# Kernel tuning notes

Measured on AMD Instinct MI355X. Metric: run time of the kernel, lower is better.

The kernel has to match this reference:

```python
import jax, jax.numpy as jnp
import numpy as np
import itertools, string

# Weight space: 2-layer MLP params, flattened in dict-key order (W1, W2, b1, b2).
SPECS = [(0, 1), (1, 2), (1,), (2,)]
N = 1024            # size of each permutable dim (perm ids 0,1,2)
C_IN, C_OUT = 16, 16
NUM_TERMS = [9, 10, 7, 6]   # equivariant basis terms per output leaf


def _set_partitions(elems):
    if not elems:
        yield []
        return
    first, rest = elems[0], elems[1:]
    for part in _set_partitions(rest):
        for i in range(len(part)):
            yield part[:i] + [part[i] + [first]] + part[i + 1:]
        yield part + [[first]]


def gen_basis(out_spec, in_spec, out_dims, x):
    """All permutation-equivariant basis maps from x (*in_dims, c) to (*out_dims, c).
    Basis elements <-> set partitions of (in,out) axis positions sharing a perm id:
    in-axes in a block are diagonalized; in-only blocks are summed; mixed blocks copy
    the axis to the matching out position; out-only blocks broadcast."""
    pos = ([('in', a, p) for a, p in enumerate(in_spec)]
           + [('out', a, p) for a, p in enumerate(out_spec)])
    by_pid = {}
    for q in pos:
        by_pid.setdefault(q[2], []).append(q)
    parts = [list(_set_partitions(by_pid[p])) for p in sorted(by_pid)]
    terms = []
    for combo in itertools.product(*parts):
        blocks = [b for part in combo for b in part]
        pos2b = {(q[0], q[1]): bi for bi, b in enumerate(blocks) for q in b}
        L = string.ascii_lowercase
        in_sub = ''.join(L[pos2b[('in', a)]] for a in range(len(in_spec)))
        mixed = [bi for bi, b in enumerate(blocks)
                 if any(q[0] == 'in' for q in b) and any(q[0] == 'out' for q in b)]
        out_sub = ''.join(L[bi] for bi in mixed)
        # diagonal over repeated in-axes, sum over in-only blocks; z = channel axis
        t = jnp.einsum(f'{in_sub}z->{out_sub}z', x)
        targets = [min(q[1] for q in blocks[bi] if q[0] == 'out') for bi in mixed]
        t = jnp.transpose(t, list(np.argsort(targets)) + [len(mixed)])
        st = sorted(targets)
        for ax in range(len(out_dims)):
            if ax not in st:
                t = jnp.expand_dims(t, ax)
        t = jnp.broadcast_to(t, tuple(out_dims) + (x.shape[-1],))
        for b in blocks:  # diagonal-embed blocks with >1 out axis (not hit for MLP specs)
            outs = sorted(q[1] for q in b if q[0] == 'out')
            for a1, a2 in zip(outs, outs[1:]):
                n = out_dims[a1]
                sh = [1] * (len(out_dims) + 1)
                sh[a1] = n; sh[a2] = n
                t = t * jnp.eye(n, dtype=x.dtype).reshape(sh)
        terms.append(t)
    return terms


def _forward(flat, thetas, biases):
    outs = []
    for i in range(len(flat)):
        out_dims = flat[i].shape[:-1]
        acc = jnp.zeros(tuple(out_dims) + (C_OUT,), dtype=flat[i].dtype)
        k = 0
        for j in range(len(flat)):
            for term in gen_basis(SPECS[i], SPECS[j], out_dims, flat[j]):
                acc = acc + jnp.einsum('...i,io->...o', term, thetas[i][k])
                k += 1
        outs.append(acc + biases[i])
    return tuple(outs)


def setup_inputs() -> dict:
    key = jax.random.key(0)
    ks = jax.random.split(key, 12)
    inp = {
        'W1': jax.random.normal(ks[0], (N, N, C_IN), jnp.float32),
        'W2': jax.random.normal(ks[1], (N, N, C_IN), jnp.float32),
        'b1': jax.random.normal(ks[2], (N, C_IN), jnp.float32),
        'b2': jax.random.normal(ks[3], (N, C_IN), jnp.float32),
    }
    for i, k in enumerate(NUM_TERMS):
        scale = (1.0 / (C_IN * k)) ** 0.5
        inp[f'theta_{i}'] = scale * jax.random.normal(ks[4 + i], (k, C_IN, C_OUT), jnp.float32)
        inp[f'bias_{i}'] = jnp.zeros((C_OUT,), jnp.float32)
    return inp


def reference(W1, W2, b1, b2, theta_0, theta_1, theta_2, theta_3,
              bias_0, bias_1, bias_2, bias_3):
    return _forward([W1, W2, b1, b2],
                    [theta_0, theta_1, theta_2, theta_3],
                    [bias_0, bias_1, bias_2, bias_3])
```

## Files before the change

### kernel.cpp

```cpp
#include <hip/hip_runtime.h>

#define NDIM 1024
#define CH 16
#define ROW_FLOATS (NDIM * CH)
#define ROW_F4 (ROW_FLOATS / 4)

__device__ inline float4 f4add(float4 a, float4 b) {
    return make_float4(a.x + b.x, a.y + b.y, a.z + b.z, a.w + b.w);
}

__global__ __launch_bounds__(256) void k_fused(const float* __restrict__ W1,
                                               const float* __restrict__ W2,
                                               float* __restrict__ rowpart,
                                               float* __restrict__ colpart) {
    int t  = threadIdx.x;
    int jt = blockIdx.x, it = blockIdx.y, z = blockIdx.z;
    int i0 = it * 16, j0 = jt * 64;
    const float4* Wf4 = (const float4*)(z ? W2 : W1);
    const float4* base = Wf4 + (size_t)i0 * ROW_F4 + jt * 256 + t;

    __shared__ float4 tile[16][257];
    float4 colacc = make_float4(0.f, 0.f, 0.f, 0.f);
#pragma unroll
    for (int r = 0; r < 16; ++r) {
        float4 v = base[(size_t)r * ROW_F4];
        colacc = f4add(colacc, v);
        tile[r][t] = v;
    }
    ((float4*)colpart)[(((size_t)z * 64 + it) * NDIM + j0) * 4 + t] = colacc;
    __syncthreads();
    if (t < 64) {
        int r = t >> 2, cq = t & 3;
        float4 s = make_float4(0.f, 0.f, 0.f, 0.f);
#pragma unroll
        for (int jl = 0; jl < 64; ++jl) s = f4add(s, tile[r][jl * 4 + cq]);
        ((float4*)rowpart)[(((size_t)z * 16 + jt) * NDIM + (i0 + r)) * 4 + cq] = s;
    }
}

__global__ __launch_bounds__(256) void k_finalize(const float* __restrict__ rowpart,
                                                  const float* __restrict__ colpart,
                                                  float* __restrict__ rowsumF,
                                                  float* __restrict__ colsumF) {
    int gt = blockIdx.x * 256 + threadIdx.x;
    if (gt < 32768) {
        int z = gt >> 14, idx = gt & 16383;
        const float* p = rowpart + (size_t)z * 16 * 16384 + idx;
        float s = 0.f;
#pragma unroll
        for (int c = 0; c < 16; ++c) s += p[(size_t)c * 16384];
        rowsumF[gt] = s;
    } else {
        int rem = gt - 32768;
        int z = rem >> 14, idx = rem & 16383;
        const float* p = colpart + (size_t)z * 64 * 16384 + idx;
        float s = 0.f;
#pragma unroll
        for (int c = 0; c < 64; ++c) s += p[(size_t)c * 16384];
        colsumF[rem] = s;
    }
}

__global__ __launch_bounds__(256) void k_sums(const float* __restrict__ rowsum,
                                              const float* __restrict__ b1,
                                              const float* __restrict__ b2,
                                              float* __restrict__ sums) {
    int tgt = blockIdx.x;
    const float* src = (tgt == 0) ? rowsum
                     : (tgt == 1) ? rowsum + 16384
                     : (tgt == 2) ? b1 : b2;
    int t = threadIdx.x;
    const float4* s4 = (const float4*)src;
    float4 a = make_float4(0.f, 0.f, 0.f, 0.f);
#pragma unroll
    for (int k = 0; k < 16; ++k) a = f4add(a, s4[t + 256 * k]);
    __shared__ float4 lds[256];
    lds[t] = a;
    __syncthreads();
    if (t < 64) {
        float4 s = lds[t];
#pragma unroll
        for (int o = 1; o < 4; ++o) s = f4add(s, lds[t + 64 * o]);
        lds[t] = s;
    }
    __syncthreads();
    if (t < 4) {
        float4 s = make_float4(0.f, 0.f, 0.f, 0.f);
#pragma unroll
        for (int m = 0; m < 16; ++m) s = f4add(s, lds[t + 4 * m]);
        float* dst = sums + tgt * 16 + 4 * t;
        dst[0] = s.x; dst[1] = s.y; dst[2] = s.z; dst[3] = s.w;
    }
}

__global__ __launch_bounds__(256) void k_smalls(const float* __restrict__ rowsum,
                                                const float* __restrict__ colsum,
                                                const float* __restrict__ sums,
                                                const float* __restrict__ b1,
                                                const float* __restrict__ b2,
                                                const float* __restrict__ th0,
                                                const float* __restrict__ th1,
                                                const float* __restrict__ th2,
                                                const float* __restrict__ th3,
                                                const float* __restrict__ bias0,
                                                const float* __restrict__ bias1,
                                                const float* __restrict__ bias2,
                                                const float* __restrict__ bias3,
                                                float* __restrict__ R0, float* __restrict__ C0,
                                                float* __restrict__ R1, float* __restrict__ C1,
                                                float* __restrict__ out2, float* __restrict__ out3) {
    int gt = blockIdx.x * 256 + threadIdx.x;
    int i = gt >> 4, o = gt & 15;
    const float* rs1 = rowsum + i * 16;
    const float* rs2 = rowsum + 16384 + i * 16;
    const float* cs1 = colsum + i * 16;
    const float* cs2 = colsum + 16384 + i * 16;
    const float* b1i = b1 + i * 16;
    const float* b2i = b2 + i * 16;
    float r0 = 0.f, c0a = 0.f, r1 = 0.f, c1a = 0.f, o2 = 0.f, o3 = 0.f;
    float k0 = 0.f, k1 = 0.f, k2 = 0.f, k3 = 0.f;
#pragma unroll
    for (int c = 0; c < 16; ++c) {
        float sW1 = sums[c], sW2 = sums[16 + c], sb1 = sums[32 + c], sb2 = sums[48 + c];
        r0  += rs1[c] * th0[(1 * 16 + c) * 16 + o];
        c0a += cs1[c] * th0[(2 * 16 + c) * 16 + o]
             + rs2[c] * th0[(4 * 16 + c) * 16 + o]
             + b1i[c] * th0[(6 * 16 + c) * 16 + o];
        k0  += sW1 * th0[(3 * 16 + c) * 16 + o] + sW2 * th0[(5 * 16 + c) * 16 + o]
             + sb1 * th0[(7 * 16 + c) * 16 + o] + sb2 * th0[(8 * 16 + c) * 16 + o];
        r1  += cs1[c] * th1[(0 * 16 + c) * 16 + o]
             + rs2[c] * th1[(3 * 16 + c) * 16 + o]
             + b1i[c] * th1[(6 * 16 + c) * 16 + o];
        c1a += cs2[c] * th1[(4 * 16 + c) * 16 + o]
             + b2i[c] * th1[(8 * 16 + c) * 16 + o];
        k1  += sW1 * th1[(1 * 16 + c) * 16 + o] + sW2 * th1[(5 * 16 + c) * 16 + o]
             + sb1 * th1[(7 * 16 + c) * 16 + o] + sb2 * th1[(9 * 16 + c) * 16 + o];
        o2  += cs1[c] * th2[(0 * 16 + c) * 16 + o]
             + rs2[c] * th2[(2 * 16 + c) * 16 + o]
             + b1i[c] * th2[(4 * 16 + c) * 16 + o];
        k2  += sW1 * th2[(1 * 16 + c) * 16 + o] + sW2 * th2[(3 * 16 + c) * 16 + o]
             + sb1 * th2[(5 * 16 + c) * 16 + o] + sb2 * th2[(6 * 16 + c) * 16 + o];
        o3  += cs2[c] * th3[(1 * 16 + c) * 16 + o]
             + b2i[c] * th3[(4 * 16 + c) * 16 + o];
        k3  += sW1 * th3[(0 * 16 + c) * 16 + o] + sW2 * th3[(2 * 16 + c) * 16 + o]
             + sb1 * th3[(3 * 16 + c) * 16 + o] + sb2 * th3[(5 * 16 + c) * 16 + o];
    }
    R0[gt]   = r0;
    C0[gt]   = c0a + k0 + bias0[o];
    R1[gt]   = r1;
    C1[gt]   = c1a + k1 + bias1[o];
    out2[gt] = o2 + k2 + bias2[o];
    out3[gt] = o3 + k3 + bias3[o];
}

__global__ __launch_bounds__(256) void k_main(const float* __restrict__ W1,
                                              const float* __restrict__ W2,
                                              const float* __restrict__ R0,
                                              const float* __restrict__ C0,
                                              const float* __restrict__ R1,
                                              const float* __restrict__ C1,
                                              const float* __restrict__ th0,
                                              const float* __restrict__ th1,
                                              float* __restrict__ out0,
                                              float* __restrict__ out1) {
    int z = blockIdx.z;
    const float* W  = z ? W2 : W1;
    const float* R  = z ? R1 : R0;
    const float* Cc = z ? C1 : C0;
    const float* TH = z ? th1 : th0;
    float* out      = z ? out1 : out0;

    int t = threadIdx.x;
    int i = blockIdx.y;
    int j = blockIdx.x * 256 + t;

    __shared__ float th[256];
    __shared__ float r[16];
    th[t] = TH[t];
    if (t < 16) r[t] = R[i * 16 + t];
    __syncthreads();

    size_t base = ((size_t)i * NDIM + j) * CH;
    const float4* xp = (const float4*)(W + base);
    float4 x0 = xp[0], x1 = xp[1], x2 = xp[2], x3 = xp[3];
    float x[16] = {x0.x, x0.y, x0.z, x0.w, x1.x, x1.y, x1.z, x1.w,
                   x2.x, x2.y, x2.z, x2.w, x3.x, x3.y, x3.z, x3.w};

    const float4* cj = (const float4*)(Cc + j * 16);
    float4 c0 = cj[0], c1 = cj[1], c2 = cj[2], c3 = cj[3];
    float acc[16] = {c0.x, c0.y, c0.z, c0.w, c1.x, c1.y, c1.z, c1.w,
                     c2.x, c2.y, c2.z, c2.w, c3.x, c3.y, c3.z, c3.w};
#pragma unroll
    for (int o = 0; o < 16; ++o) acc[o] += r[o];
#pragma unroll
    for (int c = 0; c < 16; ++c) {
        float xv = x[c];
#pragma unroll
        for (int o = 0; o < 16; ++o) acc[o] += xv * th[c * 16 + o];
    }
    float4* op = (float4*)(out + base);
    op[0] = make_float4(acc[0],  acc[1],  acc[2],  acc[3]);
    op[1] = make_float4(acc[4],  acc[5],  acc[6],  acc[7]);
    op[2] = make_float4(acc[8],  acc[9],  acc[10], acc[11]);
    op[3] = make_float4(acc[12], acc[13], acc[14], acc[15]);
}

extern "C" void kernel_launch(void* const* d_in, const int* in_sizes, int n_in,
                              void* d_out, int out_size, void* d_ws, size_t ws_size,
                              hipStream_t stream) {
    const float* W1    = (const float*)d_in[0];
    const float* W2    = (const float*)d_in[1];
    const float* b1    = (const float*)d_in[2];
    const float* b2    = (const float*)d_in[3];
    const float* th0   = (const float*)d_in[4];
    const float* bias0 = (const float*)d_in[5];
    const float* th1   = (const float*)d_in[6];
    const float* bias1 = (const float*)d_in[7];
    const float* th2   = (const float*)d_in[8];
    const float* bias2 = (const float*)d_in[9];
    const float* th3   = (const float*)d_in[10];
    const float* bias3 = (const float*)d_in[11];

    float* out  = (float*)d_out;
    float* out0 = out;
    float* out1 = out + (size_t)NDIM * NDIM * CH;
    float* out2 = out1 + (size_t)NDIM * NDIM * CH;
    float* out3 = out2 + (size_t)NDIM * CH;

    float* rowpart = out0;
    float* colpart = out0 + 524288;

    float* ws      = (float*)d_ws;
    float* rowsumF = ws;
    float* colsumF = ws + 32768;
    float* sums    = ws + 65536;
    float* R0      = ws + 65600;
    float* C0      = R0 + 16384;
    float* R1      = C0 + 16384;
    float* C1      = R1 + 16384;

    k_fused<<<dim3(16, 64, 2), dim3(256), 0, stream>>>(W1, W2, rowpart, colpart);
    k_finalize<<<dim3(256), dim3(256), 0, stream>>>(rowpart, colpart, rowsumF, colsumF);
    k_sums<<<dim3(4), dim3(256), 0, stream>>>(rowsumF, b1, b2, sums);
    k_smalls<<<dim3(64), dim3(256), 0, stream>>>(rowsumF, colsumF, sums, b1, b2,
                                                 th0, th1, th2, th3,
                                                 bias0, bias1, bias2, bias3,
                                                 R0, C0, R1, C1, out2, out3);
    k_main<<<dim3(4, NDIM, 2), dim3(256), 0, stream>>>(W1, W2, R0, C0, R1, C1,
                                                       th0, th1 + 2 * 256,
                                                       out0, out1);
}
```

Measured before the change: 105.5 us.

## Merge finalize/sums/smalls into one mid kernel and stage main I/O through LDS

The reduction pipeline shrinks from four kernels to two. k_fused now uses 8-row tiles and also writes per-tile totals, and a single k_mid kernel finishes the row and column reductions, computes the global sums and evaluates the small heads. k_main now loads W through padded LDS so that global loads and stores are fully coalesced, replacing the old per-thread 64-byte strided accesses. This is meant to cut launch count and improve memory coalescing. The cost is redundant global-sum loops in each k_mid block (2048-iteration serial loops) and two extra barriers in k_main.

```diff
diff --git a/kernel.cpp b/kernel.cpp
--- a/kernel.cpp
+++ b/kernel.cpp
@@ -2,119 +2,106 @@
 
 #define NDIM 1024
 #define CH 16
-#define ROW_FLOATS (NDIM * CH)
-#define ROW_F4 (ROW_FLOATS / 4)
+#define ROW_F4 4096
 
 __device__ inline float4 f4add(float4 a, float4 b) {
     return make_float4(a.x + b.x, a.y + b.y, a.z + b.z, a.w + b.w);
 }
+__device__ inline float4 f4zero() { return make_float4(0.f, 0.f, 0.f, 0.f); }
 
 __global__ __launch_bounds__(256) void k_fused(const float* __restrict__ W1,
                                                const float* __restrict__ W2,
                                                float* __restrict__ rowpart,
-                                               float* __restrict__ colpart) {
+                                               float* __restrict__ colpart,
+                                               float* __restrict__ tiletot) {
     int t  = threadIdx.x;
     int jt = blockIdx.x, it = blockIdx.y, z = blockIdx.z;
-    int i0 = it * 16, j0 = jt * 64;
-    const float4* Wf4 = (const float4*)(z ? W2 : W1);
-    const float4* base = Wf4 + (size_t)i0 * ROW_F4 + jt * 256 + t;
-
-    __shared__ float4 tile[16][257];
-    float4 colacc = make_float4(0.f, 0.f, 0.f, 0.f);
-#pragma unroll
-    for (int r = 0; r < 16; ++r) {
+    const float4* base = (const float4*)(z ? W2 : W1)
+                       + (size_t)it * 8 * ROW_F4 + jt * 256 + t;
+    __shared__ float4 tile[8][258];
+    __shared__ float4 rtot[32];
+    float4 colacc = f4zero();
+#pragma unroll
+    for (int r = 0; r < 8; ++r) {
         float4 v = base[(size_t)r * ROW_F4];
         colacc = f4add(colacc, v);
         tile[r][t] = v;
     }
-    ((float4*)colpart)[(((size_t)z * 64 + it) * NDIM + j0) * 4 + t] = colacc;
-    __syncthreads();
-    if (t < 64) {
+    ((float4*)colpart)[(size_t)(z * 128 + it) * 4096 + jt * 256 + t] = colacc;
+    __syncthreads();
+    if (t < 32) {
         int r = t >> 2, cq = t & 3;
-        float4 s = make_float4(0.f, 0.f, 0.f, 0.f);
+        float4 s = f4zero();
 #pragma unroll
         for (int jl = 0; jl < 64; ++jl) s = f4add(s, tile[r][jl * 4 + cq]);
-        ((float4*)rowpart)[(((size_t)z * 16 + jt) * NDIM + (i0 + r)) * 4 + cq] = s;
-    }
-}
-
-__global__ __launch_bounds__(256) void k_finalize(const float* __restrict__ rowpart,
-                                                  const float* __restrict__ colpart,
-                                                  float* __restrict__ rowsumF,
-                                                  float* __restrict__ colsumF) {
-    int gt = blockIdx.x * 256 + threadIdx.x;
-    if (gt < 32768) {
-        int z = gt >> 14, idx = gt & 16383;
-        const float* p = rowpart + (size_t)z * 16 * 16384 + idx;
+        ((float4*)rowpart)[(size_t)(z * 16 + jt) * 4096 + (it * 8 + r) * 4 + cq] = s;
+        rtot[t] = s;
+    }
+    __syncthreads();
+    if (t < 4) {
+        float4 s = f4zero();
+#pragma unroll
+        for (int r = 0; r < 8; ++r) s = f4add(s, rtot[r * 4 + t]);
+        ((float4*)tiletot)[(size_t)(z * 2048 + it * 16 + jt) * 4 + t] = s;
+    }
+}
+
+__global__ __launch_bounds__(256) void k_mid(const float* __restrict__ rowpart,
+                                             const float* __restrict__ colpart,
+                                             const float* __restrict__ tiletot,
+                                             const float* __restrict__ b1,
+                                             const float* __restrict__ b2,
+                                             const float* __restrict__ th0,
+                                             const float* __restrict__ th1,
+                                             const float* __restrict__ th2,
+                                             const float* __restrict__ th3,
+                                             const float* __restrict__ bias0,
+                                             const float* __restrict__ bias1,
+                                             const float* __restrict__ bias2,
+                                             const float* __restrict__ bias3,
+                                             float* __restrict__ R0, float* __restrict__ C0,
+                                             float* __restrict__ R1, float* __restrict__ C1,
+                                             float* __restrict__ out2, float* __restrict__ out3) {
+    int t  = threadIdx.x;
+    int i0 = blockIdx.x * 16;
+    __shared__ float sums[64];
+    __shared__ float Ars1[16][16], Ars2[16][16], Acs1[16][16], Acs2[16][16];
+
+    if (t < 32) {
+        int z = t >> 4, c = t & 15;
         float s = 0.f;
-#pragma unroll
-        for (int c = 0; c < 16; ++c) s += p[(size_t)c * 16384];
-        rowsumF[gt] = s;
-    } else {
-        int rem = gt - 32768;
-        int z = rem >> 14, idx = rem & 16383;
-        const float* p = colpart + (size_t)z * 64 * 16384 + idx;
+        for (int k = 0; k < 2048; ++k) s += tiletot[(size_t)(z * 2048 + k) * 16 + c];
+        sums[z * 16 + c] = s;
+    } else if (t < 64) {
+        int w = (t - 32) >> 4, c = t & 15;
+        const float* b = w ? b2 : b1;
         float s = 0.f;
-#pragma unroll
-        for (int c = 0; c < 64; ++c) s += p[(size_t)c * 16384];
-        colsumF[rem] = s;
-    }
-}
-
-__global__ __launch_bounds__(256) void k_sums(const float* __restrict__ rowsum,
-                                              const float* __restrict__ b1,
-                                              const float* __restrict__ b2,
-                                              float* __restrict__ sums) {
-    int tgt = blockIdx.x;
-    const float* src = (tgt == 0) ? rowsum
-                     : (tgt == 1) ? rowsum + 16384
-                     : (tgt == 2) ? b1 : b2;
-    int t = threadIdx.x;
-    const float4* s4 = (const float4*)src;
-    float4 a = make_float4(0.f, 0.f, 0.f, 0.f);
-#pragma unroll
-    for (int k = 0; k < 16; ++k) a = f4add(a, s4[t + 256 * k]);
-    __shared__ float4 lds[256];
-    lds[t] = a;
-    __syncthreads();
-    if (t < 64) {
-        float4 s = lds[t];
-#pragma unroll
-        for (int o = 1; o < 4; ++o) s = f4add(s, lds[t + 64 * o]);
-        lds[t] = s;
-    }
-    __syncthreads();
-    if (t < 4) {
-        float4 s = make_float4(0.f, 0.f, 0.f, 0.f);
-#pragma unroll
-        for (int m = 0; m < 16; ++m) s = f4add(s, lds[t + 4 * m]);
-        float* dst = sums + tgt * 16 + 4 * t;
-        dst[0] = s.x; dst[1] = s.y; dst[2] = s.z; dst[3] = s.w;
-    }
-}
-
-__global__ __launch_bounds__(256) void k_smalls(const float* __restrict__ rowsum,
-                                                const float* __restrict__ colsum,
-                                                const float* __restrict__ sums,
-                                                const float* __restrict__ b1,
-                                                const float* __restrict__ b2,
-                                                const float* __restrict__ th0,
-                                                const float* __restrict__ th1,
-                                                const float* __restrict__ th2,
-                                                const float* __restrict__ th3,
-                                                const float* __restrict__ bias0,
-                                                const float* __restrict__ bias1,
-                                                const float* __restrict__ bias2,
-                                                const float* __restrict__ bias3,
-                                                float* __restrict__ R0, float* __restrict__ C0,
-                                                float* __restrict__ R1, float* __restrict__ C1,
-                                                float* __restrict__ out2, float* __restrict__ out3) {
-    int gt = blockIdx.x * 256 + threadIdx.x;
-    int i = gt >> 4, o = gt & 15;
-    const float* rs1 = rowsum + i * 16;
-    const float* rs2 = rowsum + 16384 + i * 16;
-    const float* cs1 = colsum + i * 16;
-    const float* cs2 = colsum + 16384 + i * 16;
+        for (int k = 0; k < 1024; ++k) s += b[k * 16 + c];
+        sums[32 + w * 16 + c] = s;
+    }
+
+    {
+        int il = t >> 4, c = t & 15, i = i0 + il;
+        float s = 0.f;
+#pragma unroll 4
+        for (int k = 0; k < 16; ++k)  s += rowpart[((size_t)k * 1024 + i) * 16 + c];
+        Ars1[il][c] = s;
+        s = 0.f;
+#pragma unroll 4
+        for (int k = 0; k < 16; ++k)  s += rowpart[((size_t)(16 + k) * 1024 + i) * 16 + c];
+        Ars2[il][c] = s;
+        s = 0.f;
+#pragma unroll 8
+        for (int k = 0; k < 128; ++k) s += colpart[((size_t)k * 1024 + i) * 16 + c];
+        Acs1[il][c] = s;
+        s = 0.f;
+#pragma unroll 8
+        for (int k = 0; k < 128; ++k) s += colpart[((size_t)(128 + k) * 1024 + i) * 16 + c];
+        Acs2[il][c] = s;
+    }
+    __syncthreads();
+
+    int il = t >> 4, o = t & 15, i = i0 + il;
     const float* b1i = b1 + i * 16;
     const float* b2i = b2 + i * 16;
     float r0 = 0.f, c0a = 0.f, r1 = 0.f, c1a = 0.f, o2 = 0.f, o3 = 0.f;
@@ -122,29 +109,33 @@
 #pragma unroll
     for (int c = 0; c < 16; ++c) {
         float sW1 = sums[c], sW2 = sums[16 + c], sb1 = sums[32 + c], sb2 = sums[48 + c];
-        r0  += rs1[c] * th0[(1 * 16 + c) * 16 + o];
-        c0a += cs1[c] * th0[(2 * 16 + c) * 16 + o]
-             + rs2[c] * th0[(4 * 16 + c) * 16 + o]
-             + b1i[c] * th0[(6 * 16 + c) * 16 + o];
+        float rs1 = Ars1[il][c], rs2 = Ars2[il][c];
+        float cs1 = Acs1[il][c], cs2 = Acs2[il][c];
+        float vb1 = b1i[c], vb2 = b2i[c];
+        r0  += rs1 * th0[(1 * 16 + c) * 16 + o];
+        c0a += cs1 * th0[(2 * 16 + c) * 16 + o]
+             + rs2 * th0[(4 * 16 + c) * 16 + o]
+             + vb1 * th0[(6 * 16 + c) * 16 + o];
         k0  += sW1 * th0[(3 * 16 + c) * 16 + o] + sW2 * th0[(5 * 16 + c) * 16 + o]
              + sb1 * th0[(7 * 16 + c) * 16 + o] + sb2 * th0[(8 * 16 + c) * 16 + o];
-        r1  += cs1[c] * th1[(0 * 16 + c) * 16 + o]
-             + rs2[c] * th1[(3 * 16 + c) * 16 + o]
-             + b1i[c] * th1[(6 * 16 + c) * 16 + o];
-        c1a += cs2[c] * th1[(4 * 16 + c) * 16 + o]
-             + b2i[c] * th1[(8 * 16 + c) * 16 + o];
+        r1  += cs1 * th1[(0 * 16 + c) * 16 + o]
+             + rs2 * th1[(3 * 16 + c) * 16 + o]
+             + vb1 * th1[(6 * 16 + c) * 16 + o];
+        c1a += cs2 * th1[(4 * 16 + c) * 16 + o]
+             + vb2 * th1[(8 * 16 + c) * 16 + o];
         k1  += sW1 * th1[(1 * 16 + c) * 16 + o] + sW2 * th1[(5 * 16 + c) * 16 + o]
              + sb1 * th1[(7 * 16 + c) * 16 + o] + sb2 * th1[(9 * 16 + c) * 16 + o];
-        o2  += cs1[c] * th2[(0 * 16 + c) * 16 + o]
-             + rs2[c] * th2[(2 * 16 + c) * 16 + o]
-             + b1i[c] * th2[(4 * 16 + c) * 16 + o];
+        o2  += cs1 * th2[(0 * 16 + c) * 16 + o]
+             + rs2 * th2[(2 * 16 + c) * 16 + o]
+             + vb1 * th2[(4 * 16 + c) * 16 + o];
         k2  += sW1 * th2[(1 * 16 + c) * 16 + o] + sW2 * th2[(3 * 16 + c) * 16 + o]
              + sb1 * th2[(5 * 16 + c) * 16 + o] + sb2 * th2[(6 * 16 + c) * 16 + o];
-        o3  += cs2[c] * th3[(1 * 16 + c) * 16 + o]
-             + b2i[c] * th3[(4 * 16 + c) * 16 + o];
+        o3  += cs2 * th3[(1 * 16 + c) * 16 + o]
+             + vb2 * th3[(4 * 16 + c) * 16 + o];
         k3  += sW1 * th3[(0 * 16 + c) * 16 + o] + sW2 * th3[(2 * 16 + c) * 16 + o]
              + sb1 * th3[(3 * 16 + c) * 16 + o] + sb2 * th3[(5 * 16 + c) * 16 + o];
     }
+    int gt = i * 16 + o;
     R0[gt]   = r0;
     C0[gt]   = c0a + k0 + bias0[o];
     R1[gt]   = r1;
@@ -170,23 +161,33 @@
     const float* TH = z ? th1 : th0;
     float* out      = z ? out1 : out0;
 
-    int t = threadIdx.x;
-    int i = blockIdx.y;
-    int j = blockIdx.x * 256 + t;
-
-    __shared__ float th[256];
-    __shared__ float r[16];
+    int t  = threadIdx.x;
+    int i  = blockIdx.y;
+    int jb = blockIdx.x * 256;
+
+    __shared__ float4 xs[1280];
+    __shared__ float  th[256];
+    __shared__ float  r[16];
     th[t] = TH[t];
     if (t < 16) r[t] = R[i * 16 + t];
-    __syncthreads();
-
-    size_t base = ((size_t)i * NDIM + j) * CH;
-    const float4* xp = (const float4*)(W + base);
-    float4 x0 = xp[0], x1 = xp[1], x2 = xp[2], x3 = xp[3];
-    float x[16] = {x0.x, x0.y, x0.z, x0.w, x1.x, x1.y, x1.z, x1.w,
-                   x2.x, x2.y, x2.z, x2.w, x3.x, x3.y, x3.z, x3.w};
-
-    const float4* cj = (const float4*)(Cc + j * 16);
+
+    const float4* Wf4 = (const float4*)W + (size_t)i * 4096 + jb * 4;
+    float4*       Of4 = (float4*)out    + (size_t)i * 4096 + jb * 4;
+
+#pragma unroll
+    for (int q = 0; q < 4; ++q) {
+        int g = t + 256 * q;
+        xs[5 * (g >> 2) + (g & 3)] = Wf4[g];
+    }
+    __syncthreads();
+
+    float x[16];
+#pragma unroll
+    for (int k = 0; k < 4; ++k) {
+        float4 v = xs[5 * t + k];
+        x[4 * k] = v.x; x[4 * k + 1] = v.y; x[4 * k + 2] = v.z; x[4 * k + 3] = v.w;
+    }
+    const float4* cj = (const float4*)(Cc + (jb + t) * 16);
     float4 c0 = cj[0], c1 = cj[1], c2 = cj[2], c3 = cj[3];
     float acc[16] = {c0.x, c0.y, c0.z, c0.w, c1.x, c1.y, c1.z, c1.w,
                      c2.x, c2.y, c2.z, c2.w, c3.x, c3.y, c3.z, c3.w};
@@ -198,11 +199,17 @@
 #pragma unroll
         for (int o = 0; o < 16; ++o) acc[o] += xv * th[c * 16 + o];
     }
-    float4* op = (float4*)(out + base);
-    op[0] = make_float4(acc[0],  acc[1],  acc[2],  acc[3]);
-    op[1] = make_float4(acc[4],  acc[5],  acc[6],  acc[7]);
-    op[2] = make_float4(acc[8],  acc[9],  acc[10], acc[11]);
-    op[3] = make_float4(acc[12], acc[13], acc[14], acc[15]);
+    __syncthreads();
+#pragma unroll
+    for (int k = 0; k < 4; ++k)
+        xs[5 * t + k] = make_float4(acc[4 * k], acc[4 * k + 1],
+                                    acc[4 * k + 2], acc[4 * k + 3]);
+    __syncthreads();
+#pragma unroll
+    for (int q = 0; q < 4; ++q) {
+        int g = t + 256 * q;
+        Of4[g] = xs[5 * (g >> 2) + (g & 3)];
+    }
 }
 
 extern "C" void kernel_launch(void* const* d_in, const int* in_sizes, int n_in,
@@ -229,23 +236,19 @@
 
     float* rowpart = out0;
     float* colpart = out0 + 524288;
-
-    float* ws      = (float*)d_ws;
-    float* rowsumF = ws;
-    float* colsumF = ws + 32768;
-    float* sums    = ws + 65536;
-    float* R0      = ws + 65600;
-    float* C0      = R0 + 16384;
-    float* R1      = C0 + 16384;
-    float* C1      = R1 + 16384;
-
-    k_fused<<<dim3(16, 64, 2), dim3(256), 0, stream>>>(W1, W2, rowpart, colpart);
-    k_finalize<<<dim3(256), dim3(256), 0, stream>>>(rowpart, colpart, rowsumF, colsumF);
-    k_sums<<<dim3(4), dim3(256), 0, stream>>>(rowsumF, b1, b2, sums);
-    k_smalls<<<dim3(64), dim3(256), 0, stream>>>(rowsumF, colsumF, sums, b1, b2,
-                                                 th0, th1, th2, th3,
-                                                 bias0, bias1, bias2, bias3,
-                                                 R0, C0, R1, C1, out2, out3);
+    float* tiletot = out0 + 4718592;
+
+    float* ws = (float*)d_ws;
+    float* R0 = ws;
+    float* C0 = R0 + 16384;
+    float* R1 = C0 + 16384;
+    float* C1 = R1 + 16384;
+
+    k_fused<<<dim3(16, 128, 2), dim3(256), 0, stream>>>(W1, W2, rowpart, colpart, tiletot);
+    k_mid<<<dim3(64), dim3(256), 0, stream>>>(rowpart, colpart, tiletot, b1, b2,
+                                              th0, th1, th2, th3,
+                                              bias0, bias1, bias2, bias3,
+                                              R0, C0, R1, C1, out2, out3);
     k_main<<<dim3(4, NDIM, 2), dim3(256), 0, stream>>>(W1, W2, R0, C0, R1, C1,
                                                        th0, th1 + 2 * 256,
                                                        out0, out1);
```

Result: slower. 163.2 us (+54.7%).
